# Kernel optimization log

Hardware: AMD Instinct MI355X
Metric: run time of the kernel (lower is better)

## Reference

```python
import jax, jax.numpy as jnp
import numpy as np

INPUT_DIM = 512
D_KQ = 64
D_V = 64
SEQ = 8192


def setup_inputs() -> dict:
    key = jax.random.key(0)
    k_x, k_q, k_k, k_v = jax.random.split(key, 4)
    x = jax.random.normal(k_x, (SEQ, INPUT_DIM), dtype=jnp.float32)
    # Original uses torch.rand (uniform [0,1)) for the parameters.
    W_query = jax.random.uniform(k_q, (INPUT_DIM, D_KQ), dtype=jnp.float32)
    W_key = jax.random.uniform(k_k, (INPUT_DIM, D_KQ), dtype=jnp.float32)
    W_value = jax.random.uniform(k_v, (INPUT_DIM, D_V), dtype=jnp.float32)
    return {"x": x, "W_query": W_query, "W_key": W_key, "W_value": W_value}


def reference(x, W_query, W_key, W_value):
    # Full-recompute path of AttentionOptimized: single-head attention.
    Q = x @ W_query          # [T, d_kq]
    K = x @ W_key            # [T, d_kq]
    V = x @ W_value          # [T, d_v]
    scale = jnp.asarray(D_KQ, x.dtype) ** 0.5
    scores = Q @ K.T         # [T, T]
    attn = jax.nn.softmax(scores / scale, axis=-1)
    return attn @ V          # [T, d_v]
```

## Files before the change

kernel.cpp:

```cpp
#include <hip/hip_runtime.h>
#include <hip/hip_bf16.h>
#include <math.h>

#define SEQ 8192
#define DIN 512
#define DH  64
#define SG  8
#define CHUNK (SEQ / SG)
#define BK  64
#define NIT (CHUNK / BK)
#define LDP 72
#define SXP 516

typedef float f32x4 __attribute__((ext_vector_type(4)));
typedef short short8 __attribute__((ext_vector_type(8)));
typedef ushort us4 __attribute__((ext_vector_type(4)));

static __device__ __forceinline__ ushort bf16_of(float v) {
  __hip_bfloat16 h = __float2bfloat16(v);
  return *reinterpret_cast<ushort*>(&h);
}
static __device__ __forceinline__ float f_of_bf16(ushort u) {
  __hip_bfloat16 h;
  *reinterpret_cast<ushort*>(&h) = u;
  return __bfloat162float(h);
}
static __device__ __forceinline__ f32x4 mfma16(short8 a, short8 b, f32x4 c) {
  return __builtin_amdgcn_mfma_f32_16x16x32_bf16(a, b, c, 0, 0, 0);
}
static __device__ __forceinline__ uint pack_bf16(float a, float b) {
  __hip_bfloat162 h2 = __float22bfloat162_rn(make_float2(a, b));
  return *reinterpret_cast<uint*>(&h2);
}
static __device__ __forceinline__ int slot_of(int p) {
  return ((((p >> 2) & 1) * 2 + (p >> 5)) << 4) | (((p >> 3) & 3) << 2) | (p & 3);
}

__global__ __launch_bounds__(256, 2) void pgemm_kernel(
    const float* __restrict__ x,  const float* __restrict__ Wq,
    const float* __restrict__ Wk, const float* __restrict__ Wv,
    ushort* __restrict__ Qh, ushort* __restrict__ Ql,
    ushort* __restrict__ Kh, ushort* __restrict__ Kl,
    ushort* __restrict__ Vt) {
  __shared__ float sx[16][SXP];
  float* mb = &sx[0][0];

  const int tid = threadIdx.x;
  const int wv = tid >> 6, lane = tid & 63;
  const int ln = lane & 15, qd = lane >> 4;
  const int rb = blockIdx.x * 16;

  {
    const float4* xg = reinterpret_cast<const float4*>(x + (size_t)rb * DIN);
#pragma unroll
    for (int j = 0; j < 8; ++j) {
      const int idx = tid + 256 * j;
      const int row = idx >> 7;
      const int col = (idx & 127) * 4;
      *reinterpret_cast<float4*>(&sx[row][col]) = xg[idx];
    }
  }
  __syncthreads();

  f32x4 acc[3][4];
#pragma unroll
  for (int m = 0; m < 3; ++m)
#pragma unroll
    for (int nt = 0; nt < 4; ++nt)
#pragma unroll
      for (int i = 0; i < 4; ++i) acc[m][nt][i] = 0.f;

  const int kb = wv * 128;
  const int wbase = (kb + qd * 8) * 64 + ln;

  float wf[2][32];
#define LDW(kt_, m_, buf_)                                                     \
  do {                                                                         \
    const float* W_ = ((m_) == 0) ? Wq : (((m_) == 1) ? Wk : Wv);              \
    const int o_ = wbase + (kt_) * 32 * 64;                                    \
    _Pragma("unroll") for (int nt = 0; nt < 4; ++nt)                           \
      _Pragma("unroll") for (int j = 0; j < 8; ++j)                            \
        wf[buf_][nt * 8 + j] = W_[o_ + j * 64 + nt * 16];                      \
  } while (0)

  LDW(0, 0, 0);
#pragma unroll
  for (int kt = 0; kt < 4; ++kt) {
    const int k0 = kb + kt * 32;
    float xs[8];
    *reinterpret_cast<float4*>(xs) =
        *reinterpret_cast<const float4*>(&sx[ln][k0 + qd * 8]);
    *reinterpret_cast<float4*>(xs + 4) =
        *reinterpret_cast<const float4*>(&sx[ln][k0 + qd * 8 + 4]);
    ushort ah[8] __attribute__((aligned(16)));
    ushort al[8] __attribute__((aligned(16)));
#pragma unroll
    for (int j = 0; j < 8; ++j) {
      const ushort h = bf16_of(xs[j]);
      ah[j] = h;
      al[j] = bf16_of(xs[j] - f_of_bf16(h));
    }
    const short8 Ah = *reinterpret_cast<short8*>(ah);
    const short8 Al = *reinterpret_cast<short8*>(al);
#pragma unroll
    for (int m = 0; m < 3; ++m) {
      const int g = kt * 3 + m;
      const int buf = g & 1;
      if (g < 11) {
        const int gn = g + 1;
        LDW(gn / 3, gn % 3, buf ^ 1);
      }
      const float scale = (m == 0) ? 0.125f * 1.44269504088896f : 1.0f;
#pragma unroll
      for (int nt = 0; nt < 4; ++nt) {
        ushort bh8[8] __attribute__((aligned(16)));
        ushort bl8[8] __attribute__((aligned(16)));
#pragma unroll
        for (int j = 0; j < 8; ++j) {
          const float v = wf[buf][nt * 8 + j] * scale;
          const ushort h = bf16_of(v);
          bh8[j] = h;
          bl8[j] = bf16_of(v - f_of_bf16(h));
        }
        const short8 bh = *reinterpret_cast<short8*>(bh8);
        const short8 bl = *reinterpret_cast<short8*>(bl8);
        acc[m][nt] = mfma16(Ah, bh, acc[m][nt]);
        acc[m][nt] = mfma16(Ah, bl, acc[m][nt]);
        acc[m][nt] = mfma16(Al, bh, acc[m][nt]);
      }
    }
  }
#undef LDW

  const int eidx = (qd * 4) * 64 + ln;
  __syncthreads();
  if (wv >= 2) {
    float* b = mb + (size_t)(wv - 2) * 3072;
#pragma unroll
    for (int m = 0; m < 3; ++m)
#pragma unroll
      for (int nt = 0; nt < 4; ++nt)
#pragma unroll
        for (int r = 0; r < 4; ++r)
          b[m * 1024 + eidx + r * 64 + nt * 16] = acc[m][nt][r];
  }
  __syncthreads();
  if (wv < 2) {
    const float* b = mb + (size_t)wv * 3072;
#pragma unroll
    for (int m = 0; m < 3; ++m)
#pragma unroll
      for (int nt = 0; nt < 4; ++nt)
#pragma unroll
        for (int r = 0; r < 4; ++r)
          acc[m][nt][r] += b[m * 1024 + eidx + r * 64 + nt * 16];
  }
  __syncthreads();
  if (wv == 1) {
#pragma unroll
    for (int m = 0; m < 3; ++m)
#pragma unroll
      for (int nt = 0; nt < 4; ++nt)
#pragma unroll
        for (int r = 0; r < 4; ++r)
          mb[m * 1024 + eidx + r * 64 + nt * 16] = acc[m][nt][r];
  }
  __syncthreads();
  if (wv == 0) {
#pragma unroll
    for (int m = 0; m < 3; ++m)
#pragma unroll
      for (int nt = 0; nt < 4; ++nt)
#pragma unroll
        for (int r = 0; r < 4; ++r)
          acc[m][nt][r] += mb[m * 1024 + eidx + r * 64 + nt * 16];

#pragma unroll
    for (int m = 0; m < 2; ++m) {
      ushort* H = (m == 0) ? Qh : Kh;
      ushort* L = (m == 0) ? Ql : Kl;
#pragma unroll
      for (int nt = 0; nt < 4; ++nt)
#pragma unroll
        for (int r = 0; r < 4; ++r) {
          const float v = acc[m][nt][r];
          const int row = rb + qd * 4 + r;
          const int col = nt * 16 + ln;
          const ushort h = bf16_of(v);
          H[(size_t)row * DH + col] = h;
          L[(size_t)row * DH + col] = bf16_of(v - f_of_bf16(h));
        }
    }
#pragma unroll
    for (int nt = 0; nt < 4; ++nt) {
      ushort vp[4] __attribute__((aligned(8)));
#pragma unroll
      for (int r = 0; r < 4; ++r) vp[r] = bf16_of(acc[2][nt][r]);
      *reinterpret_cast<us4*>(Vt + (size_t)(nt * 16 + ln) * SEQ + rb + qd * 4) =
          *reinterpret_cast<us4*>(vp);
    }
  }
}

__global__ __launch_bounds__(256, 2) void flash_kernel(
    const ushort* __restrict__ Qh, const ushort* __restrict__ Ql,
    const ushort* __restrict__ Kh, const ushort* __restrict__ Kl,
    const ushort* __restrict__ Vt,
    ushort* __restrict__ Opart, float* __restrict__ Mpart,
    float* __restrict__ Lpart) {
  __shared__ __attribute__((aligned(16))) ushort sKh[2][BK][LDP];
  __shared__ __attribute__((aligned(16))) ushort sKl[2][BK][LDP];
  __shared__ __attribute__((aligned(16))) ushort sVt[2][DH][LDP];

  const int tid  = threadIdx.x;
  const int wv   = tid >> 6;
  const int lane = tid & 63;
  const int ln   = lane & 15;
  const int qd   = lane >> 4;
  const int bid  = blockIdx.x;
  const int sg   = bid & 7;
  const int qt   = bid >> 3;
  const int qrow0  = qt * 128 + wv * 32;
  const int k0base = sg * CHUNK;

  const int r0 = tid >> 3, g0 = (tid & 7) * 8;
  const int r1 = r0 + 32,  g1 = g0;
  const int sr0 = slot_of(r0), sr1 = slot_of(r1);

  const ushort one_u = (ln == 0) ? (ushort)0x3F80 : (ushort)0;
  short8 afr1;
#pragma unroll
  for (int j = 0; j < 8; ++j) afr1[j] = (short)one_u;

  short8 bqh[2][2], bql[2][2];
#pragma unroll
  for (int s = 0; s < 2; ++s)
#pragma unroll
    for (int kt = 0; kt < 2; ++kt) {
      bqh[s][kt] = *reinterpret_cast<const short8*>(
          Qh + (size_t)(qrow0 + s * 16 + ln) * DH + kt * 32 + qd * 8);
      bql[s][kt] = *reinterpret_cast<const short8*>(
          Ql + (size_t)(qrow0 + s * 16 + ln) * DH + kt * 32 + qd * 8);
    }

  f32x4 accO[2][4], accL[2];
  float m_run[2] = {-INFINITY, -INFINITY};
#pragma unroll
  for (int s = 0; s < 2; ++s) {
#pragma unroll
    for (int nt = 0; nt < 4; ++nt)
#pragma unroll
      for (int i = 0; i < 4; ++i) accO[s][nt][i] = 0.f;
#pragma unroll
    for (int i = 0; i < 4; ++i) accL[s][i] = 0.f;
  }

  uint4 pk0, pk1, pl0, pl1, pv0, pv1;
#define LOAD_TILES(k0_)                                                        \
  do {                                                                         \
    pk0 = *reinterpret_cast<const uint4*>(Kh + (size_t)((k0_) + r0) * DH + g0);\
    pk1 = *reinterpret_cast<const uint4*>(Kh + (size_t)((k0_) + r1) * DH + g1);\
    pl0 = *reinterpret_cast<const uint4*>(Kl + (size_t)((k0_) + r0) * DH + g0);\
    pl1 = *reinterpret_cast<const uint4*>(Kl + (size_t)((k0_) + r1) * DH + g1);\
    pv0 = *reinterpret_cast<const uint4*>(Vt + (size_t)r0 * SEQ + (k0_) + g0); \
    pv1 = *reinterpret_cast<const uint4*>(Vt + (size_t)r1 * SEQ + (k0_) + g1); \
  } while (0)
#define STORE_TILES(b_)                                                        \
  do {                                                                         \
    *reinterpret_cast<uint4*>(&sKh[b_][sr0][g0]) = pk0;                        \
    *reinterpret_cast<uint4*>(&sKh[b_][sr1][g1]) = pk1;                        \
    *reinterpret_cast<uint4*>(&sKl[b_][sr0][g0]) = pl0;                        \
    *reinterpret_cast<uint4*>(&sKl[b_][sr1][g1]) = pl1;                        \
    *reinterpret_cast<uint4*>(&sVt[b_][r0][g0])  = pv0;                        \
    *reinterpret_cast<uint4*>(&sVt[b_][r1][g1])  = pv1;                        \
  } while (0)

  LOAD_TILES(k0base);
  STORE_TILES(0);
  __syncthreads();

  for (int it = 0; it < NIT; ++it) {
    const int cur = it & 1;
    const int k0n = k0base + ((it + 1 < NIT) ? (it + 1) : it) * BK;
    LOAD_TILES(k0n);

    f32x4 accS[2][4];
#pragma unroll
    for (int nt = 0; nt < 4; ++nt) {
#pragma unroll
      for (int s = 0; s < 2; ++s)
#pragma unroll
        for (int i = 0; i < 4; ++i) accS[s][nt][i] = 0.f;
      const short8 kh0 = *reinterpret_cast<const short8*>(&sKh[cur][nt * 16 + ln][qd * 8]);
      const short8 kh1 = *reinterpret_cast<const short8*>(&sKh[cur][nt * 16 + ln][32 + qd * 8]);
      const short8 kl0 = *reinterpret_cast<const short8*>(&sKl[cur][nt * 16 + ln][qd * 8]);
      const short8 kl1 = *reinterpret_cast<const short8*>(&sKl[cur][nt * 16 + ln][32 + qd * 8]);
#pragma unroll
      for (int s = 0; s < 2; ++s) {
        accS[s][nt] = mfma16(kh0, bqh[s][0], accS[s][nt]);
        accS[s][nt] = mfma16(kh1, bqh[s][1], accS[s][nt]);
        accS[s][nt] = mfma16(kh0, bql[s][0], accS[s][nt]);
        accS[s][nt] = mfma16(kh1, bql[s][1], accS[s][nt]);
        accS[s][nt] = mfma16(kl0, bqh[s][0], accS[s][nt]);
        accS[s][nt] = mfma16(kl1, bqh[s][1], accS[s][nt]);
      }
    }

    uint pkd[2][4][2];
#pragma unroll
    for (int s = 0; s < 2; ++s) {
      float tmax = fmaxf(
          fmaxf(fmaxf(accS[s][0][0], accS[s][0][1]), fmaxf(accS[s][0][2], accS[s][0][3])),
          fmaxf(fmaxf(accS[s][1][0], accS[s][1][1]), fmaxf(accS[s][1][2], accS[s][1][3])));
      tmax = fmaxf(tmax, fmaxf(
          fmaxf(fmaxf(accS[s][2][0], accS[s][2][1]), fmaxf(accS[s][2][2], accS[s][2][3])),
          fmaxf(fmaxf(accS[s][3][0], accS[s][3][1]), fmaxf(accS[s][3][2], accS[s][3][3]))));
      tmax = fmaxf(tmax, __shfl_xor(tmax, 16));
      tmax = fmaxf(tmax, __shfl_xor(tmax, 32));
      const float mnew  = fmaxf(m_run[s], tmax);
      const float alpha = exp2f(m_run[s] - mnew);
      m_run[s] = mnew;
#pragma unroll
      for (int nt = 0; nt < 4; ++nt) {
        const float p0 = exp2f(accS[s][nt][0] - mnew);
        const float p1 = exp2f(accS[s][nt][1] - mnew);
        const float p2 = exp2f(accS[s][nt][2] - mnew);
        const float p3 = exp2f(accS[s][nt][3] - mnew);
        pkd[s][nt][0] = pack_bf16(p0, p1);
        pkd[s][nt][1] = pack_bf16(p2, p3);
#pragma unroll
        for (int i = 0; i < 4; ++i) accO[s][nt][i] *= alpha;
      }
      accL[s][0] *= alpha;
    }

#pragma unroll
    for (int kt2 = 0; kt2 < 2; ++kt2) {
      short8 pfrag[2];
#pragma unroll
      for (int s = 0; s < 2; ++s) {
        uint4 du;
        du.x = pkd[s][kt2][0];
        du.y = pkd[s][kt2][1];
        du.z = pkd[s][kt2 + 2][0];
        du.w = pkd[s][kt2 + 2][1];
        pfrag[s] = *reinterpret_cast<short8*>(&du);
      }
#pragma unroll
      for (int nt2 = 0; nt2 < 4; ++nt2) {
        const short8 vA = *reinterpret_cast<const short8*>(
            &sVt[cur][nt2 * 16 + ln][kt2 * 32 + qd * 8]);
        accO[0][nt2] = mfma16(vA, pfrag[0], accO[0][nt2]);
        accO[1][nt2] = mfma16(vA, pfrag[1], accO[1][nt2]);
      }
      accL[0] = mfma16(afr1, pfrag[0], accL[0]);
      accL[1] = mfma16(afr1, pfrag[1], accL[1]);
    }

    if (it + 1 < NIT) {
      STORE_TILES(cur ^ 1);
      __syncthreads();
    }
  }
#undef LOAD_TILES
#undef STORE_TILES

#pragma unroll
  for (int s = 0; s < 2; ++s) {
    const int qrow = qrow0 + s * 16 + ln;
    ushort* Ob = Opart + ((size_t)sg * SEQ + qrow) * DH;
#pragma unroll
    for (int nt = 0; nt < 4; ++nt) {
      ushort op[4] __attribute__((aligned(8)));
#pragma unroll
      for (int r = 0; r < 4; ++r) op[r] = bf16_of(accO[s][nt][r]);
      *reinterpret_cast<us4*>(Ob + nt * 16 + qd * 4) =
          *reinterpret_cast<us4*>(op);
    }
    if (qd == 0) {
      Mpart[(size_t)sg * SEQ + qrow] = m_run[s];
      Lpart[(size_t)sg * SEQ + qrow] = accL[s][0];
    }
  }
}

__global__ __launch_bounds__(256) void merge_kernel(
    const ushort* __restrict__ Opart, const float* __restrict__ Mpart,
    const float* __restrict__ Lpart, float* __restrict__ out) {
  const int idx = blockIdx.x * 256 + threadIdx.x;
  const int row = idx >> 4;
  const int c4  = (idx & 15) * 4;

  float m[SG];
  float M = -INFINITY;
#pragma unroll
  for (int i = 0; i < SG; ++i) {
    m[i] = Mpart[(size_t)i * SEQ + row];
    M = fmaxf(M, m[i]);
  }
  float L = 0.f;
  float a0 = 0.f, a1 = 0.f, a2 = 0.f, a3 = 0.f;
#pragma unroll
  for (int i = 0; i < SG; ++i) {
    const float w = exp2f(m[i] - M);
    L += w * Lpart[(size_t)i * SEQ + row];
    const us4 o = *reinterpret_cast<const us4*>(
        Opart + ((size_t)i * SEQ + row) * DH + c4);
    a0 += w * f_of_bf16(o[0]);
    a1 += w * f_of_bf16(o[1]);
    a2 += w * f_of_bf16(o[2]);
    a3 += w * f_of_bf16(o[3]);
  }
  const float rL = 1.0f / L;
  float4 res = make_float4(a0 * rL, a1 * rL, a2 * rL, a3 * rL);
  *reinterpret_cast<float4*>(out + (size_t)row * DH + c4) = res;
}

extern "C" void kernel_launch(void* const* d_in, const int* in_sizes, int n_in,
                              void* d_out, int out_size, void* d_ws, size_t ws_size,
                              hipStream_t stream) {
  const float* x  = (const float*)d_in[0];
  const float* Wq = (const float*)d_in[1];
  const float* Wk = (const float*)d_in[2];
  const float* Wv = (const float*)d_in[3];
  float* out = (float*)d_out;

  const size_t S64 = (size_t)SEQ * DH;
  ushort* Qh = (ushort*)d_ws;
  ushort* Ql = Qh + S64;
  ushort* Kh = Ql + S64;
  ushort* Kl = Kh + S64;
  ushort* Vt = Kl + S64;
  ushort* Op = Vt + S64;
  float*  Mp = (float*)(Op + (size_t)SG * S64);
  float*  Lp = Mp + (size_t)SG * SEQ;

  pgemm_kernel<<<SEQ / 16, 256, 0, stream>>>(x, Wq, Wk, Wv, Qh, Ql, Kh, Kl, Vt);
  flash_kernel<<<(SEQ / 128) * SG, 256, 0, stream>>>(Qh, Ql, Kh, Kl, Vt, Op, Mp, Lp);
  merge_kernel<<<(SEQ * 16) / 256, 256, 0, stream>>>(Op, Mp, Lp, out);
}
```

Measured before the change: 128.5 us.

## Double key-split count, XOR-swizzle shared tiles, and raise flash occupancy

```diff
diff --git a/kernel.cpp b/kernel.cpp
--- a/kernel.cpp
+++ b/kernel.cpp
@@ -5,11 +5,11 @@
 #define SEQ 8192
 #define DIN 512
 #define DH  64
-#define SG  8
+#define SG  16
 #define CHUNK (SEQ / SG)
 #define BK  64
 #define NIT (CHUNK / BK)
-#define LDP 72
+#define LDK 64
 #define SXP 516
 
 typedef float f32x4 __attribute__((ext_vector_type(4)));
@@ -34,6 +34,9 @@
 }
 static __device__ __forceinline__ int slot_of(int p) {
   return ((((p >> 2) & 1) * 2 + (p >> 5)) << 4) | (((p >> 3) & 3) << 2) | (p & 3);
+}
+static __device__ __forceinline__ int swz(int row, int col) {
+  return col ^ ((row & 7) << 3);
 }
 
 __global__ __launch_bounds__(256, 2) void pgemm_kernel(
@@ -202,15 +205,15 @@
   }
 }
 
-__global__ __launch_bounds__(256, 2) void flash_kernel(
+__global__ __launch_bounds__(256, 3) void flash_kernel(
     const ushort* __restrict__ Qh, const ushort* __restrict__ Ql,
     const ushort* __restrict__ Kh, const ushort* __restrict__ Kl,
     const ushort* __restrict__ Vt,
     ushort* __restrict__ Opart, float* __restrict__ Mpart,
     float* __restrict__ Lpart) {
-  __shared__ __attribute__((aligned(16))) ushort sKh[2][BK][LDP];
-  __shared__ __attribute__((aligned(16))) ushort sKl[2][BK][LDP];
-  __shared__ __attribute__((aligned(16))) ushort sVt[2][DH][LDP];
+  __shared__ __attribute__((aligned(16))) ushort sKh[2][BK][LDK];
+  __shared__ __attribute__((aligned(16))) ushort sKl[2][BK][LDK];
+  __shared__ __attribute__((aligned(16))) ushort sVt[2][DH][LDK];
 
   const int tid  = threadIdx.x;
   const int wv   = tid >> 6;
@@ -218,8 +221,8 @@
   const int ln   = lane & 15;
   const int qd   = lane >> 4;
   const int bid  = blockIdx.x;
-  const int sg   = bid & 7;
-  const int qt   = bid >> 3;
+  const int sg   = bid & (SG - 1);
+  const int qt   = bid / SG;
   const int qrow0  = qt * 128 + wv * 32;
   const int k0base = sg * CHUNK;
 
@@ -267,12 +270,12 @@
   } while (0)
 #define STORE_TILES(b_)                                                        \
   do {                                                                         \
-    *reinterpret_cast<uint4*>(&sKh[b_][sr0][g0]) = pk0;                        \
-    *reinterpret_cast<uint4*>(&sKh[b_][sr1][g1]) = pk1;                        \
-    *reinterpret_cast<uint4*>(&sKl[b_][sr0][g0]) = pl0;                        \
-    *reinterpret_cast<uint4*>(&sKl[b_][sr1][g1]) = pl1;                        \
-    *reinterpret_cast<uint4*>(&sVt[b_][r0][g0])  = pv0;                        \
-    *reinterpret_cast<uint4*>(&sVt[b_][r1][g1])  = pv1;                        \
+    *reinterpret_cast<uint4*>(&sKh[b_][sr0][swz(sr0, g0)]) = pk0;              \
+    *reinterpret_cast<uint4*>(&sKh[b_][sr1][swz(sr1, g1)]) = pk1;              \
+    *reinterpret_cast<uint4*>(&sKl[b_][sr0][swz(sr0, g0)]) = pl0;              \
+    *reinterpret_cast<uint4*>(&sKl[b_][sr1][swz(sr1, g1)]) = pl1;              \
+    *reinterpret_cast<uint4*>(&sVt[b_][r0][swz(r0, g0)])   = pv0;              \
+    *reinterpret_cast<uint4*>(&sVt[b_][r1][swz(r1, g1)])   = pv1;              \
   } while (0)
 
   LOAD_TILES(k0base);
@@ -291,10 +294,11 @@
       for (int s = 0; s < 2; ++s)
 #pragma unroll
         for (int i = 0; i < 4; ++i) accS[s][nt][i] = 0.f;
-      const short8 kh0 = *reinterpret_cast<const short8*>(&sKh[cur][nt * 16 + ln][qd * 8]);
-      const short8 kh1 = *reinterpret_cast<const short8*>(&sKh[cur][nt * 16 + ln][32 + qd * 8]);
-      const short8 kl0 = *reinterpret_cast<const short8*>(&sKl[cur][nt * 16 + ln][qd * 8]);
-      const short8 kl1 = *reinterpret_cast<const short8*>(&sKl[cur][nt * 16 + ln][32 + qd * 8]);
+      const int kr = nt * 16 + ln;
+      const short8 kh0 = *reinterpret_cast<const short8*>(&sKh[cur][kr][swz(kr, qd * 8)]);
+      const short8 kh1 = *reinterpret_cast<const short8*>(&sKh[cur][kr][swz(kr, 32 + qd * 8)]);
+      const short8 kl0 = *reinterpret_cast<const short8*>(&sKl[cur][kr][swz(kr, qd * 8)]);
+      const short8 kl1 = *reinterpret_cast<const short8*>(&sKl[cur][kr][swz(kr, 32 + qd * 8)]);
 #pragma unroll
       for (int s = 0; s < 2; ++s) {
         accS[s][nt] = mfma16(kh0, bqh[s][0], accS[s][nt]);
@@ -348,8 +352,9 @@
       }
 #pragma unroll
       for (int nt2 = 0; nt2 < 4; ++nt2) {
+        const int vr = nt2 * 16 + ln;
         const short8 vA = *reinterpret_cast<const short8*>(
-            &sVt[cur][nt2 * 16 + ln][kt2 * 32 + qd * 8]);
+            &sVt[cur][vr][swz(vr, kt2 * 32 + qd * 8)]);
         accO[0][nt2] = mfma16(vA, pfrag[0], accO[0][nt2]);
         accO[1][nt2] = mfma16(vA, pfrag[1], accO[1][nt2]);
       }
```

Result: slower. 137.9 us (+7.4%).
